# Optimization experiments

Hardware: AMD Instinct MI355X
Metric: run time of the kernel (lower is better)

## Reference

```python
import jax, jax.numpy as jnp
import numpy as np

B, S, D, H = 4, 4096, 1024, 1024


def log_g(x):
    # where(x >= 0, log(relu(x) + 0.5), -softplus(-x)); relu(x)+0.5 >= 0.5 so log is safe
    return jnp.where(x >= 0, jnp.log(jax.nn.relu(x) + 0.5), -jax.nn.softplus(-x))


def setup_inputs() -> dict:
    key = jax.random.key(0)
    ks = jax.random.split(key, 8)
    scale = 1.0 / np.sqrt(D)
    return {
        "x_t": jax.random.normal(ks[0], (B, S, D), dtype=jnp.float32),
        "pre_h": jax.random.normal(ks[1], (B, 1, H), dtype=jnp.float32),
        "W_f": jax.random.uniform(ks[2], (H, D), jnp.float32, -scale, scale),
        "b_f": jax.random.uniform(ks[3], (H,), jnp.float32, -scale, scale),
        "W_i": jax.random.uniform(ks[4], (H, D), jnp.float32, -scale, scale),
        "b_i": jax.random.uniform(ks[5], (H,), jnp.float32, -scale, scale),
        "W_h": jax.random.uniform(ks[6], (H, D), jnp.float32, -scale, scale),
        "b_h": jax.random.uniform(ks[7], (H,), jnp.float32, -scale, scale),
    }


def reference(x_t, pre_h, W_f, b_f, W_i, b_i, W_h, b_h):
    sp = jax.nn.softplus
    f_pre = jnp.einsum("bsd,hd->bsh", x_t, W_f) + b_f
    i_pre = jnp.einsum("bsd,hd->bsh", x_t, W_i) + b_i
    h_pre = jnp.einsum("bsd,hd->bsh", x_t, W_h) + b_h

    diff = sp(-f_pre) - sp(-i_pre)
    log_f = -sp(diff)        # (B, S, H)
    log_i = -sp(-diff)       # (B, S, H)

    log_h0 = log_g(pre_h)                 # (B, 1, H)
    log_tilde_h = log_g(h_pre)            # (B, S, H)
    log_values = jnp.concatenate([log_h0, log_i + log_tilde_h], axis=1)  # (B, S+1, H)

    # parallel_scan_log: pad cumsum at END of seq dim (as in source: F.pad(..., (0,0,0,1)))
    a_star = jnp.pad(jnp.cumsum(log_f, axis=1), ((0, 0), (0, 1), (0, 0)))  # (B, S+1, H)
    log_h0_plus_b_star = jax.lax.cumlogsumexp(log_values - a_star, axis=1)
    log_h = a_star + log_h0_plus_b_star
    return jnp.exp(log_h)[:, 1:]  # (B, S, H)
```

## Files before the change

kernel.cpp:

```cpp
#include <hip/hip_runtime.h>
#include <hip/hip_bf16.h>
#include <math.h>

#define B_DIM 4
#define S_DIM 4096
#define K_DIM 1024
#define H_DIM 1024
#define M_DIM (B_DIM * S_DIM)

#define BMT 128
#define BNT 64
#define KT_ITERS (K_DIM / 32)

#define NCHUNK 64
#define CLEN (S_DIM / NCHUNK)

typedef __attribute__((ext_vector_type(8))) _Float16 f16x8;
typedef __attribute__((ext_vector_type(4))) _Float16 f16x4;
typedef __attribute__((ext_vector_type(4))) float f32x4;

__device__ __forceinline__ float sp_f(float x) {
    return fmaxf(x, 0.0f) + __logf(1.0f + __expf(-fabsf(x)));
}
__device__ __forceinline__ float log_g_f(float x) {
    return (x >= 0.0f) ? __logf(x + 0.5f) : -sp_f(-x);
}
__device__ __forceinline__ float logaddexp_f(float a, float b) {
    float m = fmaxf(a, b);
    return m + __logf(1.0f + __expf(-fabsf(a - b)));
}
__device__ __forceinline__ float exp_sat(float x) {
    return __expf(fminf(x, 85.0f));
}

__device__ __forceinline__ void gl_lds16(const void* g, void* l) {
    __builtin_amdgcn_global_load_lds(
        (const __attribute__((address_space(1))) unsigned int*)g,
        (__attribute__((address_space(3))) unsigned int*)l, 16, 0, 0);
}

__global__ __launch_bounds__(256) void conv_f16(
    const float* __restrict__ src, _Float16* __restrict__ dst, int n4)
{
    int i = blockIdx.x * 256 + threadIdx.x;
    if (i >= n4) return;
    float4 v = ((const float4*)src)[i];
    f16x4 o = {(_Float16)v.x, (_Float16)v.y, (_Float16)v.z, (_Float16)v.w};
    ((f16x4*)dst)[i] = o;
}

__global__ __launch_bounds__(256, 2) void gemm3(
    const _Float16* __restrict__ xh,
    const _Float16* __restrict__ wh,
    const float* __restrict__ bfp, const float* __restrict__ bip,
    const float* __restrict__ bhp,
    _Float16* __restrict__ lf_out, _Float16* __restrict__ w_out)
{
    __shared__ __align__(16) char smem0[20480];
    __shared__ __align__(16) char smem1[20480];
    __shared__ __align__(16) char smem2[20480];

    const int tid = threadIdx.x;
    const int lane = tid & 63;
    const int wv = tid >> 6;
    const int wm = wv >> 1;
    const int wn = wv & 1;

    const int row0 = blockIdx.y * BMT;
    const int col0 = blockIdx.x * BNT;

    const int arow = tid & 127, akq = tid >> 7;
    unsigned ga0 = (unsigned)(((row0 + arow) * K_DIM + akq * 8) * 2);
    const int brow = tid & 63, bkq = tid >> 6;
    unsigned gb0 = (unsigned)(((0 * H_DIM + col0 + brow) * K_DIM + bkq * 8) * 2);
    unsigned gb1 = (unsigned)(((1 * H_DIM + col0 + brow) * K_DIM + bkq * 8) * 2);
    unsigned gb2 = (unsigned)(((2 * H_DIM + col0 + brow) * K_DIM + bkq * 8) * 2);

    const char* __restrict__ px = (const char*)xh;
    const char* __restrict__ pw = (const char*)wh;

    int aoff[4], boff[2];
#pragma unroll
    for (int mi = 0; mi < 4; ++mi)
        aoff[mi] = ((lane >> 4) << 11) + ((wm * 64 + mi * 16 + (lane & 15)) << 4);
#pragma unroll
    for (int nj = 0; nj < 2; ++nj)
        boff[nj] = ((lane >> 4) << 10) + ((wn * 32 + nj * 16 + (lane & 15)) << 4);

    f32x4 acc[3][4][2];
#pragma unroll
    for (int g = 0; g < 3; ++g)
#pragma unroll
        for (int mi = 0; mi < 4; ++mi)
#pragma unroll
            for (int nj = 0; nj < 2; ++nj)
                acc[g][mi][nj] = (f32x4){0.f, 0.f, 0.f, 0.f};

#define PREFETCH(nb) do { \
    gl_lds16(px + ga0,      (nb) + tid * 16); \
    gl_lds16(px + ga0 + 32, (nb) + 4096 + tid * 16); \
    gl_lds16(pw + gb0, (nb) + 8192  + tid * 16); \
    gl_lds16(pw + gb1, (nb) + 12288 + tid * 16); \
    gl_lds16(pw + gb2, (nb) + 16384 + tid * 16); \
    ga0 += 64; gb0 += 64; gb1 += 64; gb2 += 64; \
    __builtin_amdgcn_sched_barrier(0); } while (0)

#define COMPUTE(sb) do { \
    f16x8 a_[4]; \
    _Pragma("unroll") \
    for (int mi = 0; mi < 4; ++mi) \
        a_[mi] = *(const f16x8*)((sb) + aoff[mi]); \
    _Pragma("unroll") \
    for (int g = 0; g < 3; ++g) { \
        const char* bb_ = (sb) + 8192 + g * 4096; \
        f16x8 b0_ = *(const f16x8*)(bb_ + boff[0]); \
        f16x8 b1_ = *(const f16x8*)(bb_ + boff[1]); \
        _Pragma("unroll") \
        for (int mi = 0; mi < 4; ++mi) { \
            acc[g][mi][0] = __builtin_amdgcn_mfma_f32_16x16x32_f16(a_[mi], b0_, acc[g][mi][0], 0, 0, 0); \
            acc[g][mi][1] = __builtin_amdgcn_mfma_f32_16x16x32_f16(a_[mi], b1_, acc[g][mi][1], 0, 0, 0); \
        } \
    } } while (0)

#define SLOT_WAIT do { \
    asm volatile("s_waitcnt vmcnt(5) lgkmcnt(0)" ::: "memory"); \
    __builtin_amdgcn_s_barrier(); } while (0)

    PREFETCH(smem0);
    PREFETCH(smem1);
    asm volatile("s_waitcnt vmcnt(5)" ::: "memory");
    __builtin_amdgcn_s_barrier();

#pragma unroll 1
    for (int it = 0; it < (KT_ITERS - 2) / 3; ++it) {
        PREFETCH(smem2); COMPUTE(smem0); SLOT_WAIT;
        PREFETCH(smem0); COMPUTE(smem1); SLOT_WAIT;
        PREFETCH(smem1); COMPUTE(smem2); SLOT_WAIT;
    }
    COMPUTE(smem0);
    asm volatile("s_waitcnt vmcnt(0) lgkmcnt(0)" ::: "memory");
    __builtin_amdgcn_s_barrier();
    COMPUTE(smem1);

#undef PREFETCH
#undef COMPUTE
#undef SLOT_WAIT

    int nidx[2];
    float bfv[2], biv[2], bhv[2];
#pragma unroll
    for (int nj = 0; nj < 2; ++nj) {
        nidx[nj] = col0 + wn * 32 + nj * 16 + (lane & 15);
        bfv[nj] = bfp[nidx[nj]];
        biv[nj] = bip[nidx[nj]];
        bhv[nj] = bhp[nidx[nj]];
    }
#pragma unroll
    for (int mi = 0; mi < 4; ++mi) {
#pragma unroll
        for (int r = 0; r < 4; ++r) {
            int m = row0 + wm * 64 + mi * 16 + ((lane >> 4) << 2) + r;
#pragma unroll
            for (int nj = 0; nj < 2; ++nj) {
                float f_pre = acc[0][mi][nj][r] + bfv[nj];
                float i_pre = acc[1][mi][nj][r] + biv[nj];
                float h_pre = acc[2][mi][nj][r] + bhv[nj];
                float diff = sp_f(-f_pre) - sp_f(-i_pre);
                float lfv = -sp_f(diff);
                float wv_ = -sp_f(-diff) + log_g_f(h_pre);
                size_t o = (size_t)m * H_DIM + nidx[nj];
                lf_out[o] = (_Float16)lfv;
                w_out[o] = (_Float16)wv_;
            }
        }
    }
}

__global__ __launch_bounds__(256) void scan_pass_a(
    const _Float16* __restrict__ lf, const _Float16* __restrict__ w,
    float2* __restrict__ agg)
{
    int tid = blockIdx.x * blockDim.x + threadIdx.x;
    int hq = tid & (H_DIM / 4 - 1);
    int b = (tid >> 8) & (B_DIM - 1);
    int q = tid >> 10;
    int h0 = hq * 4;

    int tstart = q * CLEN + 1;
    int tend = (q == NCHUNK - 1) ? (S_DIM - 1) : (q * CLEN + CLEN);

    size_t idx = (size_t)(b * S_DIM + tstart) * H_DIM + h0;
    float c[4] = {0.f, 0.f, 0.f, 0.f};
    float r[4] = {-INFINITY, -INFINITY, -INFINITY, -INFINITY};
#pragma unroll 4
    for (int t = tstart; t <= tend; ++t) {
        f16x4 lv = *(const f16x4*)(lf + idx);
        f16x4 wv = *(const f16x4*)(w + idx - H_DIM);
#pragma unroll
        for (int j = 0; j < 4; ++j) {
            c[j] += (float)lv[j];
            r[j] = logaddexp_f(r[j], (float)wv[j] - c[j]);
        }
        idx += H_DIM;
    }
#pragma unroll
    for (int j = 0; j < 4; ++j)
        agg[(size_t)(b * H_DIM + h0 + j) * NCHUNK + q] = make_float2(c[j], r[j]);
}

__global__ __launch_bounds__(256) void scan_pass_b(
    const _Float16* __restrict__ lf, const float* __restrict__ preh,
    const float2* __restrict__ agg, float2* __restrict__ prefix)
{
    int col = blockIdx.x * blockDim.x + threadIdx.x;
    int h = col & (H_DIM - 1);
    int b = col >> 10;

    float lf0 = (float)lf[(size_t)(b * S_DIM) * H_DIM + h];
    float C = lf0;
    float R = log_g_f(preh[b * H_DIM + h]) - lf0;
    for (int q = 0; q < NCHUNK; ++q) {
        prefix[(size_t)col * NCHUNK + q] = make_float2(C, R);
        float2 a = agg[(size_t)col * NCHUNK + q];
        float Rn = logaddexp_f(R, a.y - C);
        C += a.x;
        R = Rn;
    }
}

__global__ __launch_bounds__(256) void scan_pass_c(
    const _Float16* __restrict__ lf, const _Float16* __restrict__ w,
    const float2* __restrict__ prefix, float* __restrict__ out)
{
    int tid = blockIdx.x * blockDim.x + threadIdx.x;
    int hq = tid & (H_DIM / 4 - 1);
    int b = (tid >> 8) & (B_DIM - 1);
    int q = tid >> 10;
    int h0 = hq * 4;

    float C[4], R[4];
#pragma unroll
    for (int j = 0; j < 4; ++j) {
        float2 p = prefix[(size_t)(b * H_DIM + h0 + j) * NCHUNK + q];
        C[j] = p.x; R[j] = p.y;
    }

    int tstart = q * CLEN + 1;
    int tend = (q == NCHUNK - 1) ? (S_DIM - 1) : (q * CLEN + CLEN);

    size_t idx = (size_t)(b * S_DIM + tstart) * H_DIM + h0;
#pragma unroll 4
    for (int t = tstart; t <= tend; ++t) {
        f16x4 lv = *(const f16x4*)(lf + idx);
        f16x4 wv = *(const f16x4*)(w + idx - H_DIM);
        float4 ov;
        C[0] += (float)lv[0]; R[0] = logaddexp_f(R[0], (float)wv[0] - C[0]); ov.x = exp_sat(C[0] + R[0]);
        C[1] += (float)lv[1]; R[1] = logaddexp_f(R[1], (float)wv[1] - C[1]); ov.y = exp_sat(C[1] + R[1]);
        C[2] += (float)lv[2]; R[2] = logaddexp_f(R[2], (float)wv[2] - C[2]); ov.z = exp_sat(C[2] + R[2]);
        C[3] += (float)lv[3]; R[3] = logaddexp_f(R[3], (float)wv[3] - C[3]); ov.w = exp_sat(C[3] + R[3]);
        *(float4*)(out + idx - H_DIM) = ov;
        idx += H_DIM;
    }
    if (q == NCHUNK - 1) {
        f16x4 wv = *(const f16x4*)(w + idx - H_DIM);
        float4 ov;
        ov.x = exp_sat(logaddexp_f(R[0], (float)wv[0]));
        ov.y = exp_sat(logaddexp_f(R[1], (float)wv[1]));
        ov.z = exp_sat(logaddexp_f(R[2], (float)wv[2]));
        ov.w = exp_sat(logaddexp_f(R[3], (float)wv[3]));
        *(float4*)(out + idx - H_DIM) = ov;
    }
}

extern "C" void kernel_launch(void* const* d_in, const int* in_sizes, int n_in,
                              void* d_out, int out_size, void* d_ws, size_t ws_size,
                              hipStream_t stream) {
    const float* x    = (const float*)d_in[0];
    const float* preh = (const float*)d_in[1];
    const float* Wf   = (const float*)d_in[2];
    const float* bf   = (const float*)d_in[3];
    const float* Wi   = (const float*)d_in[4];
    const float* bi   = (const float*)d_in[5];
    const float* Wh   = (const float*)d_in[6];
    const float* bh   = (const float*)d_in[7];
    float* out = (float*)d_out;

    _Float16* xh = (_Float16*)d_ws;
    _Float16* wh = xh + (size_t)M_DIM * K_DIM;
    _Float16* lf = wh + (size_t)3 * H_DIM * K_DIM;
    _Float16* wbuf = lf + (size_t)M_DIM * H_DIM;
    float2* agg = (float2*)(wbuf + (size_t)M_DIM * H_DIM);
    float2* prefix = agg + (size_t)B_DIM * H_DIM * NCHUNK;

    conv_f16<<<(M_DIM * K_DIM / 4) / 256, 256, 0, stream>>>(x, xh, M_DIM * K_DIM / 4);
    conv_f16<<<(H_DIM * K_DIM / 4) / 256, 256, 0, stream>>>(Wf, wh, H_DIM * K_DIM / 4);
    conv_f16<<<(H_DIM * K_DIM / 4) / 256, 256, 0, stream>>>(
        Wi, wh + (size_t)H_DIM * K_DIM, H_DIM * K_DIM / 4);
    conv_f16<<<(H_DIM * K_DIM / 4) / 256, 256, 0, stream>>>(
        Wh, wh + (size_t)2 * H_DIM * K_DIM, H_DIM * K_DIM / 4);

    gemm3<<<dim3(H_DIM / BNT, M_DIM / BMT), 256, 0, stream>>>(
        xh, wh, bf, bi, bh, lf, wbuf);

    scan_pass_a<<<(B_DIM * H_DIM * NCHUNK / 4) / 256, 256, 0, stream>>>(lf, wbuf, agg);
    scan_pass_b<<<(B_DIM * H_DIM) / 256, 256, 0, stream>>>(lf, preh, agg, prefix);
    scan_pass_c<<<(B_DIM * H_DIM * NCHUNK / 4) / 256, 256, 0, stream>>>(lf, wbuf, prefix, out);
}
```

Before: 386.6 us.

## Enlarge GEMM tile to 128x128 with 8 waves, swizzled LDS, interleaved staging

Result: faster. 369.3 us (-4.5%).

```diff
diff --git a/kernel.cpp b/kernel.cpp
--- a/kernel.cpp
+++ b/kernel.cpp
@@ -9,7 +9,7 @@
 #define M_DIM (B_DIM * S_DIM)
 
 #define BMT 128
-#define BNT 64
+#define BNT 128
 #define KT_ITERS (K_DIM / 32)
 
 #define NCHUNK 64
@@ -49,43 +49,47 @@
     ((f16x4*)dst)[i] = o;
 }
 
-__global__ __launch_bounds__(256, 2) void gemm3(
+__global__ __launch_bounds__(512, 2) void gemm3(
     const _Float16* __restrict__ xh,
     const _Float16* __restrict__ wh,
     const float* __restrict__ bfp, const float* __restrict__ bip,
     const float* __restrict__ bhp,
     _Float16* __restrict__ lf_out, _Float16* __restrict__ w_out)
 {
-    __shared__ __align__(16) char smem0[20480];
-    __shared__ __align__(16) char smem1[20480];
-    __shared__ __align__(16) char smem2[20480];
+    __shared__ __align__(16) char smem0[32768];
+    __shared__ __align__(16) char smem1[32768];
+    __shared__ __align__(16) char smem2[32768];
 
     const int tid = threadIdx.x;
     const int lane = tid & 63;
     const int wv = tid >> 6;
-    const int wm = wv >> 1;
-    const int wn = wv & 1;
+    const int wm = wv >> 2;
+    const int wn = wv & 3;
 
     const int row0 = blockIdx.y * BMT;
     const int col0 = blockIdx.x * BNT;
 
-    const int arow = tid & 127, akq = tid >> 7;
-    unsigned ga0 = (unsigned)(((row0 + arow) * K_DIM + akq * 8) * 2);
-    const int brow = tid & 63, bkq = tid >> 6;
-    unsigned gb0 = (unsigned)(((0 * H_DIM + col0 + brow) * K_DIM + bkq * 8) * 2);
-    unsigned gb1 = (unsigned)(((1 * H_DIM + col0 + brow) * K_DIM + bkq * 8) * 2);
-    unsigned gb2 = (unsigned)(((2 * H_DIM + col0 + brow) * K_DIM + bkq * 8) * 2);
+    const int srow = tid >> 2;
+    const int sswz = (tid & 3) ^ ((srow >> 1) & 3);
+    unsigned ga0 = (unsigned)(((row0 + srow) * K_DIM + sswz * 8) * 2);
+    unsigned gb0 = (unsigned)(((0 * H_DIM + col0 + srow) * K_DIM + sswz * 8) * 2);
+    unsigned gb1 = (unsigned)(((1 * H_DIM + col0 + srow) * K_DIM + sswz * 8) * 2);
+    unsigned gb2 = (unsigned)(((2 * H_DIM + col0 + srow) * K_DIM + sswz * 8) * 2);
 
     const char* __restrict__ px = (const char*)xh;
     const char* __restrict__ pw = (const char*)wh;
 
     int aoff[4], boff[2];
 #pragma unroll
-    for (int mi = 0; mi < 4; ++mi)
-        aoff[mi] = ((lane >> 4) << 11) + ((wm * 64 + mi * 16 + (lane & 15)) << 4);
-#pragma unroll
-    for (int nj = 0; nj < 2; ++nj)
-        boff[nj] = ((lane >> 4) << 10) + ((wn * 32 + nj * 16 + (lane & 15)) << 4);
+    for (int mi = 0; mi < 4; ++mi) {
+        int ar = wm * 64 + mi * 16 + (lane & 15);
+        aoff[mi] = ar * 64 + ((((lane >> 4) ^ ((ar >> 1) & 3))) << 4);
+    }
+#pragma unroll
+    for (int nj = 0; nj < 2; ++nj) {
+        int bc = wn * 32 + nj * 16 + (lane & 15);
+        boff[nj] = 8192 + bc * 64 + ((((lane >> 4) ^ ((bc >> 1) & 3))) << 4);
+    }
 
     f32x4 acc[3][4][2];
 #pragma unroll
@@ -96,55 +100,81 @@
             for (int nj = 0; nj < 2; ++nj)
                 acc[g][mi][nj] = (f32x4){0.f, 0.f, 0.f, 0.f};
 
-#define PREFETCH(nb) do { \
-    gl_lds16(px + ga0,      (nb) + tid * 16); \
-    gl_lds16(px + ga0 + 32, (nb) + 4096 + tid * 16); \
-    gl_lds16(pw + gb0, (nb) + 8192  + tid * 16); \
-    gl_lds16(pw + gb1, (nb) + 12288 + tid * 16); \
-    gl_lds16(pw + gb2, (nb) + 16384 + tid * 16); \
-    ga0 += 64; gb0 += 64; gb1 += 64; gb2 += 64; \
+#define STAGE4(S) do { \
+    gl_lds16(px + ga0, (S) + tid * 16); \
+    gl_lds16(pw + gb0, (S) + 8192  + tid * 16); \
+    gl_lds16(pw + gb1, (S) + 16384 + tid * 16); \
+    gl_lds16(pw + gb2, (S) + 24576 + tid * 16); \
+    ga0 += 64; gb0 += 64; gb1 += 64; gb2 += 64; } while (0)
+
+#define LGKM0 do { \
+    asm volatile("s_waitcnt lgkmcnt(0)" ::: "memory"); \
     __builtin_amdgcn_sched_barrier(0); } while (0)
 
-#define COMPUTE(sb) do { \
-    f16x8 a_[4]; \
-    _Pragma("unroll") \
-    for (int mi = 0; mi < 4; ++mi) \
-        a_[mi] = *(const f16x8*)((sb) + aoff[mi]); \
+#define MFMA_HALF(A0, A1, MI0, MI1) do { \
+    __builtin_amdgcn_s_setprio(1); \
     _Pragma("unroll") \
     for (int g = 0; g < 3; ++g) { \
-        const char* bb_ = (sb) + 8192 + g * 4096; \
-        f16x8 b0_ = *(const f16x8*)(bb_ + boff[0]); \
-        f16x8 b1_ = *(const f16x8*)(bb_ + boff[1]); \
-        _Pragma("unroll") \
-        for (int mi = 0; mi < 4; ++mi) { \
-            acc[g][mi][0] = __builtin_amdgcn_mfma_f32_16x16x32_f16(a_[mi], b0_, acc[g][mi][0], 0, 0, 0); \
-            acc[g][mi][1] = __builtin_amdgcn_mfma_f32_16x16x32_f16(a_[mi], b1_, acc[g][mi][1], 0, 0, 0); \
-        } \
-    } } while (0)
-
-#define SLOT_WAIT do { \
-    asm volatile("s_waitcnt vmcnt(5) lgkmcnt(0)" ::: "memory"); \
+        acc[g][MI0][0] = __builtin_amdgcn_mfma_f32_16x16x32_f16(A0, b_[g][0], acc[g][MI0][0], 0, 0, 0); \
+        acc[g][MI0][1] = __builtin_amdgcn_mfma_f32_16x16x32_f16(A0, b_[g][1], acc[g][MI0][1], 0, 0, 0); \
+        acc[g][MI1][0] = __builtin_amdgcn_mfma_f32_16x16x32_f16(A1, b_[g][0], acc[g][MI1][0], 0, 0, 0); \
+        acc[g][MI1][1] = __builtin_amdgcn_mfma_f32_16x16x32_f16(A1, b_[g][1], acc[g][MI1][1], 0, 0, 0); \
+    } \
+    __builtin_amdgcn_s_setprio(0); } while (0)
+
+#define TILE(CUR, STG, DOSTAGE, VN) do { \
+    f16x8 a0_ = *(const f16x8*)((CUR) + aoff[0]); \
+    f16x8 a1_ = *(const f16x8*)((CUR) + aoff[1]); \
+    f16x8 b_[3][2]; \
+    _Pragma("unroll") \
+    for (int g = 0; g < 3; ++g) { \
+        b_[g][0] = *(const f16x8*)((CUR) + g * 8192 + boff[0]); \
+        b_[g][1] = *(const f16x8*)((CUR) + g * 8192 + boff[1]); \
+    } \
+    if (DOSTAGE) { \
+        gl_lds16(px + ga0, (STG) + tid * 16); \
+        gl_lds16(pw + gb0, (STG) + 8192 + tid * 16); \
+    } \
+    __builtin_amdgcn_sched_barrier(0); \
+    __builtin_amdgcn_s_barrier(); \
+    LGKM0; \
+    MFMA_HALF(a0_, a1_, 0, 1); \
+    __builtin_amdgcn_sched_barrier(0); \
+    __builtin_amdgcn_s_barrier(); \
+    f16x8 a2_ = *(const f16x8*)((CUR) + aoff[2]); \
+    f16x8 a3_ = *(const f16x8*)((CUR) + aoff[3]); \
+    if (DOSTAGE) { \
+        gl_lds16(pw + gb1, (STG) + 16384 + tid * 16); \
+        gl_lds16(pw + gb2, (STG) + 24576 + tid * 16); \
+        ga0 += 64; gb0 += 64; gb1 += 64; gb2 += 64; \
+    } \
+    __builtin_amdgcn_sched_barrier(0); \
+    __builtin_amdgcn_s_barrier(); \
+    LGKM0; \
+    MFMA_HALF(a2_, a3_, 2, 3); \
+    asm volatile("s_waitcnt vmcnt(" #VN ")" ::: "memory"); \
+    __builtin_amdgcn_sched_barrier(0); \
     __builtin_amdgcn_s_barrier(); } while (0)
 
-    PREFETCH(smem0);
-    PREFETCH(smem1);
-    asm volatile("s_waitcnt vmcnt(5)" ::: "memory");
+    STAGE4(smem0);
+    STAGE4(smem1);
+    asm volatile("s_waitcnt vmcnt(4)" ::: "memory");
+    __builtin_amdgcn_sched_barrier(0);
     __builtin_amdgcn_s_barrier();
 
 #pragma unroll 1
-    for (int it = 0; it < (KT_ITERS - 2) / 3; ++it) {
-        PREFETCH(smem2); COMPUTE(smem0); SLOT_WAIT;
-        PREFETCH(smem0); COMPUTE(smem1); SLOT_WAIT;
-        PREFETCH(smem1); COMPUTE(smem2); SLOT_WAIT;
-    }
-    COMPUTE(smem0);
-    asm volatile("s_waitcnt vmcnt(0) lgkmcnt(0)" ::: "memory");
-    __builtin_amdgcn_s_barrier();
-    COMPUTE(smem1);
-
-#undef PREFETCH
-#undef COMPUTE
-#undef SLOT_WAIT
+    for (int it = 0; it < 10; ++it) {
+        TILE(smem0, smem2, 1, 4);
+        TILE(smem1, smem0, 1, 4);
+        TILE(smem2, smem1, 1, 4);
+    }
+    TILE(smem0, smem2, 0, 0);
+    TILE(smem1, smem0, 0, 0);
+
+#undef TILE
+#undef MFMA_HALF
+#undef LGKM0
+#undef STAGE4
 
     int nidx[2];
     float bfv[2], biv[2], bhv[2];
@@ -299,7 +329,7 @@
     conv_f16<<<(H_DIM * K_DIM / 4) / 256, 256, 0, stream>>>(
         Wh, wh + (size_t)2 * H_DIM * K_DIM, H_DIM * K_DIM / 4);
 
-    gemm3<<<dim3(H_DIM / BNT, M_DIM / BMT), 256, 0, stream>>>(
+    gemm3<<<dim3(H_DIM / BNT, M_DIM / BMT), 512, 0, stream>>>(
         xh, wh, bf, bi, bh, lf, wbuf);
 
     scan_pass_a<<<(B_DIM * H_DIM * NCHUNK / 4) / 256, 256, 0, stream>>>(lf, wbuf, agg);
```
